# Optimization experiments

Measured on AMD Instinct MI355X. Metric: run time of the kernel, lower is better.

## Reference

```python
import jax, jax.numpy as jnp
import numpy as np

B, N, M, D = 4, 2048, 2048, 512
H, HS, OUT = 8, 64, 512


def setup_inputs() -> dict:
    key = jax.random.key(0)
    ks = jax.random.split(key, 8)
    scale = 1.0 / np.sqrt(D)
    return {
        "query": jax.random.normal(ks[0], (B, N, D), jnp.float32),
        "key": jax.random.normal(ks[1], (B, M, D), jnp.float32),
        "value": jax.random.normal(ks[2], (B, M, D), jnp.float32),
        "query_kernel": jax.random.normal(ks[3], (H, D, HS), jnp.float32) * scale,
        "key_kernel": jax.random.normal(ks[4], (H, D, HS), jnp.float32) * scale,
        "value_kernel": jax.random.normal(ks[5], (H, D, HS), jnp.float32) * scale,
        "projection_kernel": jax.random.normal(ks[6], (H, HS, OUT), jnp.float32) * (1.0 / np.sqrt(H * HS)),
        "projection_bias": jnp.zeros((OUT,), jnp.float32),
    }


def reference(query, key, value, query_kernel, key_kernel, value_kernel,
              projection_kernel, projection_bias):
    # Per-head projections: B N I , H I O -> B N H O
    q = jnp.einsum('bni,hio->bnho', query, query_kernel)
    k = jnp.einsum('bmi,hio->bmho', key, key_kernel)
    v = jnp.einsum('bmi,hio->bmho', value, value_kernel)
    q = q / jnp.sqrt(jnp.asarray(HS, q.dtype))
    # Full BHNM attention matrix (matches original unfused math)
    logits = jnp.einsum('bnho,bmho->bhnm', q, k)
    attn = jax.nn.softmax(logits, axis=-1)  # dropout=0 / inference -> identity
    mh = jnp.einsum('bhnm,bmhi->bnhi', attn, v)
    out = jnp.einsum('bnhi,hio->bno', mh, projection_kernel) + projection_bias
    return out
```

## Files before the change

kernel.cpp:

```cpp
#include <hip/hip_runtime.h>
#include <hip/hip_bf16.h>


typedef __attribute__((ext_vector_type(8))) short short8;
typedef __attribute__((ext_vector_type(4))) float f32x4;

#define MFMA16(a, b, c) __builtin_amdgcn_mfma_f32_16x16x32_bf16(a, b, c, 0, 0, 0)

__device__ __forceinline__ short f2bf(float f) {
  unsigned u = __builtin_bit_cast(unsigned, f);
  u += 0x7FFF + ((u >> 16) & 1);
  return (short)(u >> 16);
}

__device__ __forceinline__ unsigned swz(unsigned byte) {
  return byte ^ (((byte >> 7) & 7) << 4);
}


__global__ void conv_wqkv(const float* __restrict__ Wq, const float* __restrict__ Wk,
                          const float* __restrict__ Wv,
                          short* __restrict__ Oq, short* __restrict__ Ok,
                          short* __restrict__ Ov) {
  int z = blockIdx.y;
  const float* W = (z == 0) ? Wq : (z == 1) ? Wk : Wv;
  short* O = (z == 0) ? Oq : (z == 1) ? Ok : Ov;
  float scale = (z == 0) ? 0.125f : 1.0f;
  int tid = blockIdx.x * 256 + threadIdx.x;
  int n = tid >> 9, k = tid & 511;
  int h = n >> 6, hs = n & 63;
  O[tid] = f2bf(W[(h * 512 + k) * 64 + hs] * scale);
}

__global__ void conv_wp(const float* __restrict__ W, short* __restrict__ O) {
  int tid = blockIdx.x * 256 + threadIdx.x;
  int n = tid >> 9, k = tid & 511;
  O[tid] = f2bf(W[k * 512 + n]);
}


template <int MODE>
__global__ __launch_bounds__(256) void gemm128(
    const void* __restrict__ A0, const void* __restrict__ A1, const void* __restrict__ A2,
    const short* __restrict__ B0, const short* __restrict__ B1, const short* __restrict__ B2,
    void* __restrict__ O0, void* __restrict__ O1, void* __restrict__ O2,
    const float* __restrict__ bias) {
  __shared__ alignas(16) char lds[65536];
  const int z = blockIdx.z;
  const void* Ap = (z == 0) ? A0 : (z == 1) ? A1 : A2;
  const short* Bp = (z == 0) ? B0 : (z == 1) ? B1 : B2;
  void* Op = (z == 0) ? O0 : (z == 1) ? O1 : O2;

  const int tid = threadIdx.x;
  const int r0 = blockIdx.x * 128;
  const int n0 = blockIdx.y * 128;
  const int wid = tid >> 6, lane = tid & 63, g = lane >> 4, c = lane & 15;
  const int wr = wid >> 1, wc = wid & 1;
  const int srow = tid >> 3, sc8 = tid & 7;

  float4 fA[4], fB[4];
  short8 sA[4], sB[4];

  auto LOAD = [&](int ks) {
    const int k0 = ks * 64;
#pragma unroll
    for (int it = 0; it < 4; ++it) {
      int row = srow + 32 * it;
      if constexpr (MODE == 0) {
        const float* src = (const float*)Ap + (size_t)(r0 + row) * 512 + k0 + sc8 * 8;
        fA[it] = *(const float4*)(src);
        fB[it] = *(const float4*)(src + 4);
      } else {
        sA[it] = *(const short8*)((const short*)Ap + (size_t)(r0 + row) * 512 + k0 + sc8 * 8);
      }
      sB[it] = *(const short8*)(Bp + (size_t)(n0 + row) * 512 + k0 + sc8 * 8);
    }
  };
  auto WRITE = [&](int buf) {
    char* Ab = lds + buf * 16384;
    char* Bb = lds + 32768 + buf * 16384;
#pragma unroll
    for (int it = 0; it < 4; ++it) {
      int row = srow + 32 * it;
      short8 s;
      if constexpr (MODE == 0) {
        s[0] = f2bf(fA[it].x); s[1] = f2bf(fA[it].y); s[2] = f2bf(fA[it].z); s[3] = f2bf(fA[it].w);
        s[4] = f2bf(fB[it].x); s[5] = f2bf(fB[it].y); s[6] = f2bf(fB[it].z); s[7] = f2bf(fB[it].w);
      } else {
        s = sA[it];
      }
      *(short8*)(Ab + swz(row * 128 + sc8 * 16)) = s;
      *(short8*)(Bb + swz(row * 128 + sc8 * 16)) = sB[it];
    }
  };

  f32x4 acc[4][4] = {};

  LOAD(0);
  WRITE(0);
  int cur = 0;

  for (int ks = 0; ks < 8; ++ks) {
    if (ks < 7) LOAD(ks + 1);
    __syncthreads();
    const char* Ab = lds + cur * 16384;
    const char* Bb = lds + 32768 + cur * 16384;

    short8 af[4][2], bf[4][2];
#pragma unroll
    for (int mt = 0; mt < 4; ++mt)
#pragma unroll
      for (int kk = 0; kk < 2; ++kk) {
        int row = wr * 64 + mt * 16 + c;
        af[mt][kk] = *(const short8*)(Ab + swz(row * 128 + (g + 4 * kk) * 16));
      }
#pragma unroll
    for (int nt = 0; nt < 4; ++nt)
#pragma unroll
      for (int kk = 0; kk < 2; ++kk) {
        int nr = wc * 64 + nt * 16 + c;
        bf[nt][kk] = *(const short8*)(Bb + swz(nr * 128 + (g + 4 * kk) * 16));
      }
#pragma unroll
    for (int mt = 0; mt < 4; ++mt)
#pragma unroll
      for (int nt = 0; nt < 4; ++nt) {
        acc[mt][nt] = MFMA16(af[mt][0], bf[nt][0], acc[mt][nt]);
        acc[mt][nt] = MFMA16(af[mt][1], bf[nt][1], acc[mt][nt]);
      }

    if (ks < 7) { WRITE(cur ^ 1); cur ^= 1; }
  }

  if constexpr (MODE == 0) {
    short* Ob = (short*)Op;
    const bool vtrans = (z == 2);
#pragma unroll
    for (int mt = 0; mt < 4; ++mt) {
      int rowb = r0 + wr * 64 + mt * 16 + g * 4;
#pragma unroll
      for (int nt = 0; nt < 4; ++nt) {
        int col = n0 + wc * 64 + nt * 16 + c;
        int hh = col >> 6, hs = col & 63;
#pragma unroll
        for (int r = 0; r < 4; ++r) {
          int row = rowb + r;
          int bb = row >> 11, nn = row & 2047;
          size_t off = vtrans ? ((((size_t)(bb * 8 + hh)) * 64 + hs) * 2048 + nn)
                              : ((((size_t)(bb * 8 + hh)) * 2048 + nn) * 64 + hs);
          Ob[off] = f2bf(acc[mt][nt][r]);
        }
      }
    }
  } else {
    float* Of = (float*)Op;
#pragma unroll
    for (int nt = 0; nt < 4; ++nt) {
      int col = n0 + wc * 64 + nt * 16 + c;
      float bv = bias[col];
#pragma unroll
      for (int mt = 0; mt < 4; ++mt) {
        int rowb = r0 + wr * 64 + mt * 16 + g * 4;
#pragma unroll
        for (int r = 0; r < 4; ++r)
          Of[(size_t)(rowb + r) * 512 + col] = acc[mt][nt][r] + bv;
      }
    }
  }
}


__global__ __launch_bounds__(256, 4) void attn64(const short* __restrict__ Qb,
                                                 const short* __restrict__ Kb,
                                                 const short* __restrict__ Vt,
                                                 short* __restrict__ MH) {
  __shared__ alignas(16) char lds[40960];
  const int flat = blockIdx.x;
  const int xcd = flat & 7, idx = flat >> 3;
  const int bh = xcd * 4 + (idx >> 5);
  const int qt = idx & 31;
  const int b = bh >> 3, h = bh & 7;

  const int tid = threadIdx.x, wid = tid >> 6, lane = tid & 63, g = lane >> 4, c = lane & 15;
  const short* Qp = Qb + ((size_t)bh * 2048 + qt * 64) * 64;
  const short* Kp = Kb + (size_t)bh * 2048 * 64;
  const short* Vp = Vt + (size_t)bh * 64 * 2048;

  const int srow = tid >> 3, sc8 = tid & 7;

  short8 qf[2];
#pragma unroll
  for (int kk = 0; kk < 2; ++kk)
    qf[kk] = *(const short8*)(Qp + (wid * 16 + c) * 64 + g * 8 + kk * 32);

  f32x4 o[4] = {};
  float mrow[4], lrow[4];
#pragma unroll
  for (int r = 0; r < 4; ++r) { mrow[r] = -1e30f; lrow[r] = 0.f; }

  const int pbase = 32768 + wid * 2048;

  short8 kr[2], vr[2];
#pragma unroll
  for (int it = 0; it < 2; ++it) {
    int row = srow + it * 32;
    kr[it] = *(const short8*)(Kp + (size_t)row * 64 + sc8 * 8);
    vr[it] = *(const short8*)(Vp + (size_t)row * 2048 + sc8 * 8);
  }
#pragma unroll
  for (int it = 0; it < 2; ++it) {
    int row = srow + it * 32;
    *(short8*)(lds + swz(row * 128 + sc8 * 16)) = kr[it];
    *(short8*)(lds + 16384 + swz(row * 128 + sc8 * 16)) = vr[it];
  }
  int cur = 0;

  for (int kvt = 0; kvt < 32; ++kvt) {
    if (kvt < 31) {
#pragma unroll
      for (int it = 0; it < 2; ++it) {
        int row = srow + it * 32;
        kr[it] = *(const short8*)(Kp + ((size_t)(kvt + 1) * 64 + row) * 64 + sc8 * 8);
        vr[it] = *(const short8*)(Vp + (size_t)row * 2048 + (kvt + 1) * 64 + sc8 * 8);
      }
    }
    __syncthreads();
    const char* Kl = lds + cur * 8192;
    const char* Vl = lds + 16384 + cur * 8192;

    f32x4 s[4] = {};
#pragma unroll
    for (int t = 0; t < 4; ++t)
#pragma unroll
      for (int kk = 0; kk < 2; ++kk) {
        short8 kf = *(const short8*)(Kl + swz((t * 16 + c) * 128 + (g + 4 * kk) * 16));
        s[t] = MFMA16(qf[kk], kf, s[t]);
      }

#pragma unroll
    for (int r = 0; r < 4; ++r) {
      float vm = fmaxf(fmaxf(s[0][r], s[1][r]), fmaxf(s[2][r], s[3][r]));
      vm = fmaxf(vm, __shfl_xor(vm, 1));
      vm = fmaxf(vm, __shfl_xor(vm, 2));
      vm = fmaxf(vm, __shfl_xor(vm, 4));
      vm = fmaxf(vm, __shfl_xor(vm, 8));
      float mn = fmaxf(mrow[r], vm);
      float sc = __expf(mrow[r] - mn);
      float rs = 0.f;
#pragma unroll
      for (int t = 0; t < 4; ++t) {
        float p = __expf(s[t][r] - mn);
        s[t][r] = p;
        rs += p;
      }
      rs += __shfl_xor(rs, 1);
      rs += __shfl_xor(rs, 2);
      rs += __shfl_xor(rs, 4);
      rs += __shfl_xor(rs, 8);
      lrow[r] = lrow[r] * sc + rs;
      mrow[r] = mn;
#pragma unroll
      for (int t = 0; t < 4; ++t) o[t][r] *= sc;
    }

#pragma unroll
    for (int t = 0; t < 4; ++t)
#pragma unroll
      for (int r = 0; r < 4; ++r)
        *(short*)(lds + swz(pbase + (g * 4 + r) * 128 + (t * 16 + c) * 2)) = f2bf(s[t][r]);
    asm volatile("s_waitcnt lgkmcnt(0)" ::: "memory");

    short8 pa[2];
#pragma unroll
    for (int half = 0; half < 2; ++half)
      pa[half] = *(const short8*)(lds + swz(pbase + c * 128 + (g + 4 * half) * 16));
#pragma unroll
    for (int t = 0; t < 4; ++t)
#pragma unroll
      for (int half = 0; half < 2; ++half) {
        short8 vf = *(const short8*)(Vl + swz((t * 16 + c) * 128 + (g + 4 * half) * 16));
        o[t] = MFMA16(pa[half], vf, o[t]);
      }

    if (kvt < 31) {
      char* Kn = lds + (cur ^ 1) * 8192;
      char* Vn = lds + 16384 + (cur ^ 1) * 8192;
#pragma unroll
      for (int it = 0; it < 2; ++it) {
        int row = srow + it * 32;
        *(short8*)(Kn + swz(row * 128 + sc8 * 16)) = kr[it];
        *(short8*)(Vn + swz(row * 128 + sc8 * 16)) = vr[it];
      }
      cur ^= 1;
    }
  }

#pragma unroll
  for (int t = 0; t < 4; ++t)
#pragma unroll
    for (int r = 0; r < 4; ++r) {
      float val = o[t][r] / lrow[r];
      int qrow = qt * 64 + wid * 16 + g * 4 + r;
      int col = h * 64 + t * 16 + c;
      MH[((size_t)b * 2048 + qrow) * 512 + col] = f2bf(val);
    }
}


extern "C" void kernel_launch(void* const* d_in, const int* in_sizes, int n_in,
                              void* d_out, int out_size, void* d_ws, size_t ws_size,
                              hipStream_t stream) {
  const float* query = (const float*)d_in[0];
  const float* key = (const float*)d_in[1];
  const float* value = (const float*)d_in[2];
  const float* wq = (const float*)d_in[3];
  const float* wk = (const float*)d_in[4];
  const float* wv = (const float*)d_in[5];
  const float* wp = (const float*)d_in[6];
  const float* bias = (const float*)d_in[7];

  char* ws = (char*)d_ws;
  short* Wq_t = (short*)(ws + 0);
  short* Wk_t = (short*)(ws + 524288);
  short* Wv_t = (short*)(ws + 1048576);
  short* Wp_t = (short*)(ws + 1572864);
  short* Qb = (short*)(ws + 2097152);
  short* Kb = (short*)(ws + 2097152 + 8388608);
  short* Vb = (short*)(ws + 2097152 + 2 * (size_t)8388608);
  short* MH = (short*)(ws + 2097152 + 3 * (size_t)8388608);

  conv_wqkv<<<dim3(1024, 3), 256, 0, stream>>>(wq, wk, wv, Wq_t, Wk_t, Wv_t);
  conv_wp<<<1024, 256, 0, stream>>>(wp, Wp_t);
  gemm128<0><<<dim3(64, 4, 3), 256, 0, stream>>>(query, key, value, Wq_t, Wk_t, Wv_t,
                                                 Qb, Kb, Vb, nullptr);
  attn64<<<dim3(1024), 256, 0, stream>>>(Qb, Kb, Vb, MH);
  gemm128<1><<<dim3(64, 4, 1), 256, 0, stream>>>(MH, nullptr, nullptr, Wp_t, nullptr, nullptr,
                                                 d_out, nullptr, nullptr, bias);
}
```

Baseline: 260.7 us.

## Use direct global-to-LDS async loads for bf16 tiles in GEMM and attention

```diff
diff --git a/kernel.cpp b/kernel.cpp
--- a/kernel.cpp
+++ b/kernel.cpp
@@ -15,6 +15,11 @@
 
 __device__ __forceinline__ unsigned swz(unsigned byte) {
   return byte ^ (((byte >> 7) & 7) << 4);
+}
+
+__device__ __forceinline__ void gload16(const void* g, void* l) {
+  __builtin_amdgcn_global_load_lds((const __attribute__((address_space(1))) void*)g,
+                                   (__attribute__((address_space(3))) void*)l, 16, 0, 0);
 }
 
 
@@ -56,53 +61,66 @@
   const int n0 = blockIdx.y * 128;
   const int wid = tid >> 6, lane = tid & 63, g = lane >> 4, c = lane & 15;
   const int wr = wid >> 1, wc = wid & 1;
+  const int rl = lane >> 3, cl = lane & 7, scol = cl ^ rl;
   const int srow = tid >> 3, sc8 = tid & 7;
 
   float4 fA[4], fB[4];
-  short8 sA[4], sB[4];
-
-  auto LOAD = [&](int ks) {
+
+  auto LOAD_A = [&](int ks) {
     const int k0 = ks * 64;
 #pragma unroll
     for (int it = 0; it < 4; ++it) {
       int row = srow + 32 * it;
-      if constexpr (MODE == 0) {
-        const float* src = (const float*)Ap + (size_t)(r0 + row) * 512 + k0 + sc8 * 8;
-        fA[it] = *(const float4*)(src);
-        fB[it] = *(const float4*)(src + 4);
-      } else {
-        sA[it] = *(const short8*)((const short*)Ap + (size_t)(r0 + row) * 512 + k0 + sc8 * 8);
-      }
-      sB[it] = *(const short8*)(Bp + (size_t)(n0 + row) * 512 + k0 + sc8 * 8);
-    }
-  };
-  auto WRITE = [&](int buf) {
+      const float* src = (const float*)Ap + (size_t)(r0 + row) * 512 + k0 + sc8 * 8;
+      fA[it] = *(const float4*)(src);
+      fB[it] = *(const float4*)(src + 4);
+    }
+  };
+  auto WRITE_A = [&](int buf) {
     char* Ab = lds + buf * 16384;
-    char* Bb = lds + 32768 + buf * 16384;
 #pragma unroll
     for (int it = 0; it < 4; ++it) {
       int row = srow + 32 * it;
       short8 s;
-      if constexpr (MODE == 0) {
-        s[0] = f2bf(fA[it].x); s[1] = f2bf(fA[it].y); s[2] = f2bf(fA[it].z); s[3] = f2bf(fA[it].w);
-        s[4] = f2bf(fB[it].x); s[5] = f2bf(fB[it].y); s[6] = f2bf(fB[it].z); s[7] = f2bf(fB[it].w);
-      } else {
-        s = sA[it];
-      }
+      s[0] = f2bf(fA[it].x); s[1] = f2bf(fA[it].y); s[2] = f2bf(fA[it].z); s[3] = f2bf(fA[it].w);
+      s[4] = f2bf(fB[it].x); s[5] = f2bf(fB[it].y); s[6] = f2bf(fB[it].z); s[7] = f2bf(fB[it].w);
       *(short8*)(Ab + swz(row * 128 + sc8 * 16)) = s;
-      *(short8*)(Bb + swz(row * 128 + sc8 * 16)) = sB[it];
+    }
+  };
+  auto ISSUE_A = [&](int ks, int buf) {
+    char* Ab = lds + buf * 16384;
+    const int k0 = ks * 64;
+#pragma unroll
+    for (int i = 0; i < 4; ++i) {
+      int ch = wid * 4 + i;
+      int row = ch * 8 + rl;
+      gload16((const short*)Ap + (size_t)(r0 + row) * 512 + k0 + scol * 8, Ab + ch * 1024);
+    }
+  };
+  auto ISSUE_B = [&](int ks, int buf) {
+    char* Bb = lds + 32768 + buf * 16384;
+    const int k0 = ks * 64;
+#pragma unroll
+    for (int i = 0; i < 4; ++i) {
+      int ch = wid * 4 + i;
+      int row = ch * 8 + rl;
+      gload16(Bp + (size_t)(n0 + row) * 512 + k0 + scol * 8, Bb + ch * 1024);
     }
   };
 
   f32x4 acc[4][4] = {};
 
-  LOAD(0);
-  WRITE(0);
+  if constexpr (MODE == 0) { LOAD_A(0); WRITE_A(0); } else { ISSUE_A(0, 0); }
+  ISSUE_B(0, 0);
   int cur = 0;
 
   for (int ks = 0; ks < 8; ++ks) {
-    if (ks < 7) LOAD(ks + 1);
     __syncthreads();
+    if (ks < 7) {
+      ISSUE_B(ks + 1, cur ^ 1);
+      if constexpr (MODE == 1) ISSUE_A(ks + 1, cur ^ 1);
+      else LOAD_A(ks + 1);
+    }
     const char* Ab = lds + cur * 16384;
     const char* Bb = lds + 32768 + cur * 16384;
 
@@ -129,7 +147,10 @@
         acc[mt][nt] = MFMA16(af[mt][1], bf[nt][1], acc[mt][nt]);
       }
 
-    if (ks < 7) { WRITE(cur ^ 1); cur ^= 1; }
+    if constexpr (MODE == 0) {
+      if (ks < 7) WRITE_A(cur ^ 1);
+    }
+    cur ^= 1;
   }
 
   if constexpr (MODE == 0) {
@@ -186,7 +207,19 @@
   const short* Kp = Kb + (size_t)bh * 2048 * 64;
   const short* Vp = Vt + (size_t)bh * 64 * 2048;
 
-  const int srow = tid >> 3, sc8 = tid & 7;
+  const int rl = lane >> 3, cl = lane & 7, scol = cl ^ rl;
+
+  auto ISSUE_KV = [&](int kvt, int buf) {
+    char* Kd = lds + buf * 8192;
+    char* Vd = lds + 16384 + buf * 8192;
+#pragma unroll
+    for (int i = 0; i < 2; ++i) {
+      int ch = wid * 2 + i;
+      int row = ch * 8 + rl;
+      gload16(Kp + ((size_t)kvt * 64 + row) * 64 + scol * 8, Kd + ch * 1024);
+      gload16(Vp + (size_t)row * 2048 + kvt * 64 + scol * 8, Vd + ch * 1024);
+    }
+  };
 
   short8 qf[2];
 #pragma unroll
@@ -200,31 +233,12 @@
 
   const int pbase = 32768 + wid * 2048;
 
-  short8 kr[2], vr[2];
-#pragma unroll
-  for (int it = 0; it < 2; ++it) {
-    int row = srow + it * 32;
-    kr[it] = *(const short8*)(Kp + (size_t)row * 64 + sc8 * 8);
-    vr[it] = *(const short8*)(Vp + (size_t)row * 2048 + sc8 * 8);
-  }
-#pragma unroll
-  for (int it = 0; it < 2; ++it) {
-    int row = srow + it * 32;
-    *(short8*)(lds + swz(row * 128 + sc8 * 16)) = kr[it];
-    *(short8*)(lds + 16384 + swz(row * 128 + sc8 * 16)) = vr[it];
-  }
+  ISSUE_KV(0, 0);
   int cur = 0;
 
   for (int kvt = 0; kvt < 32; ++kvt) {
-    if (kvt < 31) {
-#pragma unroll
-      for (int it = 0; it < 2; ++it) {
-        int row = srow + it * 32;
-        kr[it] = *(const short8*)(Kp + ((size_t)(kvt + 1) * 64 + row) * 64 + sc8 * 8);
-        vr[it] = *(const short8*)(Vp + (size_t)row * 2048 + (kvt + 1) * 64 + sc8 * 8);
-      }
-    }
     __syncthreads();
+    if (kvt < 31) ISSUE_KV(kvt + 1, cur ^ 1);
     const char* Kl = lds + cur * 8192;
     const char* Vl = lds + 16384 + cur * 8192;
 
@@ -282,17 +296,7 @@
         o[t] = MFMA16(pa[half], vf, o[t]);
       }
 
-    if (kvt < 31) {
-      char* Kn = lds + (cur ^ 1) * 8192;
-      char* Vn = lds + 16384 + (cur ^ 1) * 8192;
-#pragma unroll
-      for (int it = 0; it < 2; ++it) {
-        int row = srow + it * 32;
-        *(short8*)(Kn + swz(row * 128 + sc8 * 16)) = kr[it];
-        *(short8*)(Vn + swz(row * 128 + sc8 * 16)) = vr[it];
-      }
-      cur ^= 1;
-    }
+    cur ^= 1;
   }
 
 #pragma unroll
```

New measurement: 261.2 us. About the same (+0.2%).
